# Kernel optimization log

Measured on AMD Instinct MI355X. Metric: run time of the kernel, lower is better.

The kernel has to match this reference:

```python
import jax, jax.numpy as jnp
import numpy as np

BATCH = 1048576
D_IN = 4        # d_in=3 spatial dims + 1 time dim
HID = 64
N_HID_STACK = 4  # hidden residual blocks after the first hidden layer
D_OUT = 3
BN_EPS = 1e-5


def _bn(x, gamma, beta):
    # BatchNorm1d in training mode: biased batch statistics over the batch axis
    mu = jnp.mean(x, axis=0)
    var = jnp.var(x, axis=0)
    return gamma * (x - mu) * jax.lax.rsqrt(var + BN_EPS) + beta


def setup_inputs() -> dict:
    key = jax.random.key(0)
    ks = jax.random.split(key, 8)
    s_in = 1.0 / np.sqrt(D_IN)
    s_h = 1.0 / np.sqrt(HID)
    return {
        "x": jax.random.normal(ks[0], (BATCH, D_IN), dtype=jnp.float32),
        "bn0_gamma": jnp.ones((D_IN,), jnp.float32),
        "bn0_beta": jnp.zeros((D_IN,), jnp.float32),
        "W0": jax.random.normal(ks[1], (D_IN, HID), jnp.float32) * s_in,
        "b0": jnp.zeros((HID,), jnp.float32),
        "gamma0": jnp.ones((HID,), jnp.float32),
        "beta0": jnp.zeros((HID,), jnp.float32),
        "W_hid": jax.random.normal(ks[2], (N_HID_STACK, HID, HID), jnp.float32) * s_h,
        "b_hid": jnp.zeros((N_HID_STACK, HID), jnp.float32),
        "gamma_hid": jnp.ones((N_HID_STACK, HID), jnp.float32),
        "beta_hid": jnp.zeros((N_HID_STACK, HID), jnp.float32),
        "Wout": jax.random.normal(ks[3], (HID, D_OUT), jnp.float32) * s_h,
        "bout": jnp.zeros((D_OUT,), jnp.float32),
    }


def reference(x, bn0_gamma, bn0_beta, W0, b0, gamma0, beta0,
              W_hid, b_hid, gamma_hid, beta_hid, Wout, bout):
    # Net.forward (u-network, single patch, batch_normalization=True, tanh):
    #   x = bn0(x)
    #   y = bn(act(Linear0(x)))                 (first hidden layer, no skip)
    #   y = bn_i(act(Linear_i(y))) + y          (residual hidden layers)
    #   y = Linear_out(y)
    h = _bn(x, bn0_gamma, bn0_beta)
    y = _bn(jnp.tanh(h @ W0 + b0), gamma0, beta0)

    def step(y, layer):
        W, b, g, be = layer
        return _bn(jnp.tanh(y @ W + b), g, be) + y, None

    y, _ = jax.lax.scan(step, y, (W_hid, b_hid, gamma_hid, beta_hid))
    return y @ Wout + bout
```

## Files before the change

kernel.cpp:

```cpp
#include <hip/hip_runtime.h>
#include <stdint.h>


#define NROWS 1048576
#define EPS 1e-5f
#define INV_B 9.5367431640625e-07f
#define LOG2E2 2.885390081777927f
#define TILES 4
#define BIGGRID 2048

typedef __attribute__((ext_vector_type(8))) short bfrag;
typedef __attribute__((ext_vector_type(4))) float facc;
typedef __attribute__((ext_vector_type(4))) float f4v;

__device__ __forceinline__ float bf2f(short s) {
  union { unsigned u; float f; } v;
  v.u = ((unsigned)(unsigned short)s) << 16;
  return v.f;
}
__device__ __forceinline__ short f2bf(float f) {
  union { float f; unsigned u; } v;
  v.f = f;
  unsigned r = v.u + 0x7FFFu + ((v.u >> 16) & 1u);
  return (short)(r >> 16);
}
__device__ __forceinline__ float tanh_fast(float x) {
  float e = __builtin_amdgcn_exp2f(x * LOG2E2);
  return 1.f - 2.f * __builtin_amdgcn_rcpf(e + 1.f);
}

template <int W>
__global__ __launch_bounds__(256) void k_reduce(const float* __restrict__ P,
                                                float* __restrict__ S,
                                                int rows_per_blk) {
  __shared__ float red[256];
  const int tid = threadIdx.x;
  const int col = tid % W;
  const int grp = tid / W;
  const int G = 256 / W;
  size_t r0 = (size_t)blockIdx.x * rows_per_blk;
  float s = 0.f;
  for (int r = grp; r < rows_per_blk; r += G) s += P[(r0 + r) * W + col];
  red[tid] = s;
  __syncthreads();
  if (tid < W) {
    float t = 0.f;
#pragma unroll 4
    for (int g = 0; g < G; ++g) t += red[g * W + tid];
    atomicAdd(&S[tid], t);
  }
}


__global__ __launch_bounds__(256) void k_stats_x(const float* __restrict__ x,
                                                 float* __restrict__ P) {
  __shared__ float red[4][8];
  const int tid = threadIdx.x;
  const int wave = tid >> 6;
  size_t base = (size_t)blockIdx.x * 1024 + tid;
  float s[4] = {0.f, 0.f, 0.f, 0.f}, q[4] = {0.f, 0.f, 0.f, 0.f};
#pragma unroll
  for (int it = 0; it < 4; ++it) {
    f4v v = *(const f4v*)(x + (base + (size_t)it * 256) * 4);
#pragma unroll
    for (int k = 0; k < 4; ++k) { s[k] += v[k]; q[k] = fmaf(v[k], v[k], q[k]); }
  }
#pragma unroll
  for (int off = 32; off > 0; off >>= 1) {
#pragma unroll
    for (int k = 0; k < 4; ++k) {
      s[k] += __shfl_xor(s[k], off);
      q[k] += __shfl_xor(q[k], off);
    }
  }
  if ((tid & 63) == 0) {
#pragma unroll
    for (int k = 0; k < 4; ++k) { red[wave][k] = s[k]; red[wave][4 + k] = q[k]; }
  }
  __syncthreads();
  if (tid < 8)
    P[blockIdx.x * 8 + tid] =
        red[0][tid] + red[1][tid] + red[2][tid] + red[3][tid];
}

__global__ __launch_bounds__(256) void k_stats_z1(
    const float* __restrict__ x, const float* __restrict__ bn0g,
    const float* __restrict__ bn0b, const float* __restrict__ W0,
    const float* __restrict__ b0, const float* __restrict__ sx,
    float* __restrict__ P) {
  __shared__ float red[2][4][64];
  const int tid = threadIdx.x;
  const int lane = tid & 63;
  const int wave = tid >> 6;
  int gw = blockIdx.x * 4 + wave;
  float sc[4], sh[4];
#pragma unroll
  for (int k = 0; k < 4; ++k) {
    float mean = sx[k] * INV_B;
    float var = fmaf(-mean, mean, sx[4 + k] * INV_B);
    float rs = rsqrtf(var + EPS);
    sc[k] = bn0g[k] * rs;
    sh[k] = fmaf(-sc[k], mean, bn0b[k]);
  }
  float w[4];
#pragma unroll
  for (int k = 0; k < 4; ++k) w[k] = W0[k * 64 + lane];
  float bj = b0[lane];
  float s = 0.f, q = 0.f;
  size_t r0 = (size_t)gw * 256;
  for (int r = 0; r < 256; ++r) {
    f4v xv = *(const f4v*)(x + (r0 + r) * 4);
    float acc = bj;
#pragma unroll
    for (int k = 0; k < 4; ++k)
      acc = fmaf(fmaf(xv[k], sc[k], sh[k]), w[k], acc);
    float z = tanh_fast(acc);
    s += z;
    q = fmaf(z, z, q);
  }
  red[0][wave][lane] = s;
  red[1][wave][lane] = q;
  __syncthreads();
  if (tid < 128) {
    int which = tid >> 6, c = tid & 63;
    P[blockIdx.x * 128 + tid] = red[which][0][c] + red[which][1][c] +
                                red[which][2][c] + red[which][3][c];
  }
}

__global__ __launch_bounds__(256) void k_prep(const float* __restrict__ Wh,
                                              short* __restrict__ WT) {
  int idx = blockIdx.x * 256 + threadIdx.x;
  int l = idx >> 12, rem = idx & 4095, k = rem >> 6, c = rem & 63;
  WT[l * 4096 + c * 64 + k] = f2bf(Wh[l * 4096 + k * 64 + c]);
}


__global__ __launch_bounds__(256, 3) void k_first(
    const float* __restrict__ x, const float* __restrict__ bn0g,
    const float* __restrict__ bn0b, const float* __restrict__ W0,
    const float* __restrict__ b0, const float* __restrict__ gamma0,
    const float* __restrict__ beta0, const float* __restrict__ sx,
    const float* __restrict__ s1, const short* __restrict__ WTb,
    const float* __restrict__ bb, float* __restrict__ P,
    short* __restrict__ Y) {
  __shared__ __align__(16) float lds_x[128 * 4];
  __shared__ __align__(16) short lds_y[128 * 72];
  __shared__ float lds_st[128];

  const int tid = threadIdx.x;
  const int lane = tid & 63;
  const int wave = tid >> 6;
  const int l15 = lane & 15;
  const int q = lane >> 4;
  const int wr = wave * 32;

  if (tid < 128) lds_st[tid] = 0.f;
  float sc0[4], sh0[4];
#pragma unroll
  for (int k = 0; k < 4; ++k) {
    float mean = sx[k] * INV_B;
    float var = fmaf(-mean, mean, sx[4 + k] * INV_B);
    float rs = rsqrtf(var + EPS);
    sc0[k] = bn0g[k] * rs;
    sh0[k] = fmaf(-sc0[k], mean, bn0b[k]);
  }
  float w0c[4];
#pragma unroll
  for (int k = 0; k < 4; ++k) w0c[k] = W0[k * 64 + lane];
  float b0c = b0[lane];
  float mean1 = s1[lane] * INV_B;
  float var1 = fmaf(-mean1, mean1, s1[64 + lane] * INV_B);
  float A1c = gamma0[lane] * rsqrtf(var1 + EPS);
  float B1c = fmaf(-A1c, mean1, beta0[lane]);
  float bbv[4];
  bfrag bwb[4][2];
#pragma unroll
  for (int nt = 0; nt < 4; ++nt) {
    bbv[nt] = bb[nt * 16 + l15];
#pragma unroll
    for (int kt = 0; kt < 2; ++kt)
      bwb[nt][kt] =
          *(const bfrag*)(WTb + (nt * 16 + l15) * 64 + kt * 32 + q * 8);
  }
  __syncthreads();

  float sAcc[4] = {0.f, 0.f, 0.f, 0.f}, qAcc[4] = {0.f, 0.f, 0.f, 0.f};
  const size_t tbase = (size_t)blockIdx.x * TILES * 128;

  f4v xp;
  if (lane < 32) xp = *(const f4v*)(x + (tbase + wr + lane) * 4);

#pragma unroll
  for (int t = 0; t < TILES; ++t) {
    const size_t r0 = tbase + (size_t)t * 128;
    if (lane < 32) *(f4v*)&lds_x[(wr + lane) * 4] = xp;
    if (t + 1 < TILES && lane < 32)
      xp = *(const f4v*)(x + (r0 + 128 + wr + lane) * 4);

    for (int e = 0; e < 32; ++e) {
      int row = wr + e;
      float acc = b0c;
#pragma unroll
      for (int k = 0; k < 4; ++k)
        acc = fmaf(fmaf(lds_x[row * 4 + k], sc0[k], sh0[k]), w0c[k], acc);
      float z = tanh_fast(acc);
      lds_y[row * 72 + lane] = f2bf(fmaf(A1c, z, B1c));
    }

    bfrag af[2][2];
#pragma unroll
    for (int mt = 0; mt < 2; ++mt)
#pragma unroll
      for (int kt = 0; kt < 2; ++kt) {
        af[mt][kt] =
            *(const bfrag*)&lds_y[(wr + mt * 16 + l15) * 72 + kt * 32 + q * 8];
        *(bfrag*)(Y + (r0 + wr + mt * 16 + l15) * 64 + kt * 32 + q * 8) =
            af[mt][kt];
      }
    facc acc2[2][4];
#pragma unroll
    for (int mt = 0; mt < 2; ++mt)
#pragma unroll
      for (int nt = 0; nt < 4; ++nt) {
        acc2[mt][nt][0] = bbv[nt]; acc2[mt][nt][1] = bbv[nt];
        acc2[mt][nt][2] = bbv[nt]; acc2[mt][nt][3] = bbv[nt];
      }
#pragma unroll
    for (int mt = 0; mt < 2; ++mt)
#pragma unroll
      for (int nt = 0; nt < 4; ++nt)
#pragma unroll
        for (int kt = 0; kt < 2; ++kt)
          acc2[mt][nt] = __builtin_amdgcn_mfma_f32_16x16x32_bf16(
              af[mt][kt], bwb[nt][kt], acc2[mt][nt], 0, 0, 0);
#pragma unroll
    for (int nt = 0; nt < 4; ++nt)
#pragma unroll
      for (int mt = 0; mt < 2; ++mt)
#pragma unroll
        for (int i = 0; i < 4; ++i) {
          float z = tanh_fast(acc2[mt][nt][i]);
          sAcc[nt] += z;
          qAcc[nt] = fmaf(z, z, qAcc[nt]);
        }
  }

#pragma unroll
  for (int nt = 0; nt < 4; ++nt) {
    float s = sAcc[nt], ss = qAcc[nt];
    s += __shfl_xor(s, 16); s += __shfl_xor(s, 32);
    ss += __shfl_xor(ss, 16); ss += __shfl_xor(ss, 32);
    if (q == 0) {
      atomicAdd(&lds_st[nt * 16 + l15], s);
      atomicAdd(&lds_st[64 + nt * 16 + l15], ss);
    }
  }
  __syncthreads();
  if (tid < 128) P[(size_t)blockIdx.x * 128 + tid] = lds_st[tid];
}

__global__ __launch_bounds__(256, 3) void k_mid(
    short* __restrict__ Y, const short* __restrict__ WTa,
    const float* __restrict__ ba, const float* __restrict__ ga,
    const float* __restrict__ bea, const float* __restrict__ sa,
    const short* __restrict__ WTb, const float* __restrict__ bb,
    float* __restrict__ P) {
  __shared__ __align__(16) short lds_y[128 * 72];
  __shared__ float lds_st[128];

  const int tid = threadIdx.x;
  const int lane = tid & 63;
  const int wave = tid >> 6;
  const int l15 = lane & 15;
  const int q = lane >> 4;
  const int wr = wave * 32;

  if (tid < 128) lds_st[tid] = 0.f;
  float Av[4], Bv[4], bav[4], bbv[4];
#pragma unroll
  for (int nt = 0; nt < 4; ++nt) {
    int c = nt * 16 + l15;
    float mean = sa[c] * INV_B;
    float var = fmaf(-mean, mean, sa[64 + c] * INV_B);
    float A = ga[c] * rsqrtf(var + EPS);
    Av[nt] = A;
    Bv[nt] = fmaf(-A, mean, bea[c]);
    bav[nt] = ba[c];
    bbv[nt] = bb[c];
  }
  bfrag bwa[4][2], bwb[4][2];
#pragma unroll
  for (int nt = 0; nt < 4; ++nt)
#pragma unroll
    for (int kt = 0; kt < 2; ++kt) {
      bwa[nt][kt] =
          *(const bfrag*)(WTa + (nt * 16 + l15) * 64 + kt * 32 + q * 8);
      bwb[nt][kt] =
          *(const bfrag*)(WTb + (nt * 16 + l15) * 64 + kt * 32 + q * 8);
    }
  __syncthreads();

  float sAcc[4] = {0.f, 0.f, 0.f, 0.f}, qAcc[4] = {0.f, 0.f, 0.f, 0.f};
  const size_t tbase = (size_t)blockIdx.x * TILES * 128;
  const int srow = lane >> 3;
  const int sc8 = (lane & 7) * 8;

  bfrag ld[4];
  {
    const size_t g = (tbase + wr + srow) * 64 + sc8;
#pragma unroll
    for (int it = 0; it < 4; ++it)
      ld[it] = *(const bfrag*)(Y + g + (size_t)it * 8 * 64);
  }

#pragma unroll
  for (int t = 0; t < TILES; ++t) {
    const size_t r0 = tbase + (size_t)t * 128;
#pragma unroll
    for (int it = 0; it < 4; ++it)
      *(bfrag*)&lds_y[(wr + it * 8 + srow) * 72 + sc8] = ld[it];
    if (t + 1 < TILES) {
      const size_t g = (r0 + 128 + wr + srow) * 64 + sc8;
#pragma unroll
      for (int it = 0; it < 4; ++it)
        ld[it] = *(const bfrag*)(Y + g + (size_t)it * 8 * 64);
    }

    bfrag af[2][2];
#pragma unroll
    for (int mt = 0; mt < 2; ++mt)
#pragma unroll
      for (int kt = 0; kt < 2; ++kt)
        af[mt][kt] =
            *(const bfrag*)&lds_y[(wr + mt * 16 + l15) * 72 + kt * 32 + q * 8];
    facc acc[2][4];
#pragma unroll
    for (int mt = 0; mt < 2; ++mt)
#pragma unroll
      for (int nt = 0; nt < 4; ++nt) {
        acc[mt][nt][0] = bav[nt]; acc[mt][nt][1] = bav[nt];
        acc[mt][nt][2] = bav[nt]; acc[mt][nt][3] = bav[nt];
      }
#pragma unroll
    for (int mt = 0; mt < 2; ++mt)
#pragma unroll
      for (int nt = 0; nt < 4; ++nt)
#pragma unroll
        for (int kt = 0; kt < 2; ++kt)
          acc[mt][nt] = __builtin_amdgcn_mfma_f32_16x16x32_bf16(
              af[mt][kt], bwa[nt][kt], acc[mt][nt], 0, 0, 0);

#pragma unroll
    for (int mt = 0; mt < 2; ++mt)
#pragma unroll
      for (int nt = 0; nt < 4; ++nt) {
        int c = nt * 16 + l15;
        float A = Av[nt], Bc = Bv[nt];
#pragma unroll
        for (int i = 0; i < 4; ++i) {
          int rl = wr + mt * 16 + q * 4 + i;
          float z = tanh_fast(acc[mt][nt][i]);
          float yo = bf2f(lds_y[rl * 72 + c]);
          lds_y[rl * 72 + c] = f2bf(fmaf(A, z, Bc) + yo);
        }
      }

#pragma unroll
    for (int mt = 0; mt < 2; ++mt)
#pragma unroll
      for (int kt = 0; kt < 2; ++kt) {
        af[mt][kt] =
            *(const bfrag*)&lds_y[(wr + mt * 16 + l15) * 72 + kt * 32 + q * 8];
        *(bfrag*)(Y + (r0 + wr + mt * 16 + l15) * 64 + kt * 32 + q * 8) =
            af[mt][kt];
      }
#pragma unroll
    for (int mt = 0; mt < 2; ++mt)
#pragma unroll
      for (int nt = 0; nt < 4; ++nt) {
        acc[mt][nt][0] = bbv[nt]; acc[mt][nt][1] = bbv[nt];
        acc[mt][nt][2] = bbv[nt]; acc[mt][nt][3] = bbv[nt];
      }
#pragma unroll
    for (int mt = 0; mt < 2; ++mt)
#pragma unroll
      for (int nt = 0; nt < 4; ++nt)
#pragma unroll
        for (int kt = 0; kt < 2; ++kt)
          acc[mt][nt] = __builtin_amdgcn_mfma_f32_16x16x32_bf16(
              af[mt][kt], bwb[nt][kt], acc[mt][nt], 0, 0, 0);
#pragma unroll
    for (int nt = 0; nt < 4; ++nt)
#pragma unroll
      for (int mt = 0; mt < 2; ++mt)
#pragma unroll
        for (int i = 0; i < 4; ++i) {
          float z = tanh_fast(acc[mt][nt][i]);
          sAcc[nt] += z;
          qAcc[nt] = fmaf(z, z, qAcc[nt]);
        }
  }

#pragma unroll
  for (int nt = 0; nt < 4; ++nt) {
    float s = sAcc[nt], ss = qAcc[nt];
    s += __shfl_xor(s, 16); s += __shfl_xor(s, 32);
    ss += __shfl_xor(ss, 16); ss += __shfl_xor(ss, 32);
    if (q == 0) {
      atomicAdd(&lds_st[nt * 16 + l15], s);
      atomicAdd(&lds_st[64 + nt * 16 + l15], ss);
    }
  }
  __syncthreads();
  if (tid < 128) P[(size_t)blockIdx.x * 128 + tid] = lds_st[tid];
}

__global__ __launch_bounds__(256, 3) void k_last(
    const short* __restrict__ Y, const short* __restrict__ WTa,
    const float* __restrict__ ba, const float* __restrict__ ga,
    const float* __restrict__ bea, const float* __restrict__ sa,
    const float* __restrict__ Wout, const float* __restrict__ bout,
    float* __restrict__ out) {
  __shared__ __align__(16) short lds_y[128 * 72];
  __shared__ float lds_wo[192];

  const int tid = threadIdx.x;
  const int lane = tid & 63;
  const int wave = tid >> 6;
  const int l15 = lane & 15;
  const int q = lane >> 4;
  const int wr = wave * 32;

  if (tid < 192) lds_wo[tid] = Wout[tid];
  float Av[4], Bv[4], bav[4];
#pragma unroll
  for (int nt = 0; nt < 4; ++nt) {
    int c = nt * 16 + l15;
    float mean = sa[c] * INV_B;
    float var = fmaf(-mean, mean, sa[64 + c] * INV_B);
    float A = ga[c] * rsqrtf(var + EPS);
    Av[nt] = A;
    Bv[nt] = fmaf(-A, mean, bea[c]);
    bav[nt] = ba[c];
  }
  bfrag bwa[4][2];
#pragma unroll
  for (int nt = 0; nt < 4; ++nt)
#pragma unroll
    for (int kt = 0; kt < 2; ++kt)
      bwa[nt][kt] =
          *(const bfrag*)(WTa + (nt * 16 + l15) * 64 + kt * 32 + q * 8);
  float bo0 = bout[0], bo1 = bout[1], bo2 = bout[2];
  __syncthreads();

  const size_t tbase = (size_t)blockIdx.x * TILES * 128;
  const int srow = lane >> 3;
  const int sc8 = (lane & 7) * 8;

  bfrag ld[4];
  {
    const size_t g = (tbase + wr + srow) * 64 + sc8;
#pragma unroll
    for (int it = 0; it < 4; ++it)
      ld[it] = *(const bfrag*)(Y + g + (size_t)it * 8 * 64);
  }

#pragma unroll
  for (int t = 0; t < TILES; ++t) {
    const size_t r0 = tbase + (size_t)t * 128;
#pragma unroll
    for (int it = 0; it < 4; ++it)
      *(bfrag*)&lds_y[(wr + it * 8 + srow) * 72 + sc8] = ld[it];
    if (t + 1 < TILES) {
      const size_t g = (r0 + 128 + wr + srow) * 64 + sc8;
#pragma unroll
      for (int it = 0; it < 4; ++it)
        ld[it] = *(const bfrag*)(Y + g + (size_t)it * 8 * 64);
    }

    bfrag af[2][2];
#pragma unroll
    for (int mt = 0; mt < 2; ++mt)
#pragma unroll
      for (int kt = 0; kt < 2; ++kt)
        af[mt][kt] =
            *(const bfrag*)&lds_y[(wr + mt * 16 + l15) * 72 + kt * 32 + q * 8];
    facc acc[2][4];
#pragma unroll
    for (int mt = 0; mt < 2; ++mt)
#pragma unroll
      for (int nt = 0; nt < 4; ++nt) {
        acc[mt][nt][0] = bav[nt]; acc[mt][nt][1] = bav[nt];
        acc[mt][nt][2] = bav[nt]; acc[mt][nt][3] = bav[nt];
      }
#pragma unroll
    for (int mt = 0; mt < 2; ++mt)
#pragma unroll
      for (int nt = 0; nt < 4; ++nt)
#pragma unroll
        for (int kt = 0; kt < 2; ++kt)
          acc[mt][nt] = __builtin_amdgcn_mfma_f32_16x16x32_bf16(
              af[mt][kt], bwa[nt][kt], acc[mt][nt], 0, 0, 0);
#pragma unroll
    for (int mt = 0; mt < 2; ++mt)
#pragma unroll
      for (int nt = 0; nt < 4; ++nt) {
        int c = nt * 16 + l15;
        float A = Av[nt], Bc = Bv[nt];
#pragma unroll
        for (int i = 0; i < 4; ++i) {
          int rl = wr + mt * 16 + q * 4 + i;
          float z = tanh_fast(acc[mt][nt][i]);
          float yo = bf2f(lds_y[rl * 72 + c]);
          lds_y[rl * 72 + c] = f2bf(fmaf(A, z, Bc) + yo);
        }
      }

    {
      int row = wr + (lane >> 1);
      int cb = (lane & 1) * 32;
      float o0 = 0.f, o1 = 0.f, o2 = 0.f;
#pragma unroll
      for (int jc = 0; jc < 4; ++jc) {
        bfrag v = *(const bfrag*)&lds_y[row * 72 + cb + jc * 8];
#pragma unroll
        for (int j = 0; j < 8; ++j) {
          float f = bf2f(v[j]);
          int jj = cb + jc * 8 + j;
          o0 = fmaf(f, lds_wo[jj * 3 + 0], o0);
          o1 = fmaf(f, lds_wo[jj * 3 + 1], o1);
          o2 = fmaf(f, lds_wo[jj * 3 + 2], o2);
        }
      }
      o0 += __shfl_xor(o0, 1);
      o1 += __shfl_xor(o1, 1);
      o2 += __shfl_xor(o2, 1);
      if ((lane & 1) == 0) {
        size_t ro = (r0 + row) * 3;
        out[ro] = o0 + bo0;
        out[ro + 1] = o1 + bo1;
        out[ro + 2] = o2 + bo2;
      }
    }
  }
}

extern "C" void kernel_launch(void* const* d_in, const int* in_sizes, int n_in,
                              void* d_out, int out_size, void* d_ws,
                              size_t ws_size, hipStream_t stream) {
  (void)in_sizes; (void)n_in; (void)out_size; (void)ws_size;
  const float* x = (const float*)d_in[0];
  const float* bn0g = (const float*)d_in[1];
  const float* bn0b = (const float*)d_in[2];
  const float* W0 = (const float*)d_in[3];
  const float* b0 = (const float*)d_in[4];
  const float* gamma0 = (const float*)d_in[5];
  const float* beta0 = (const float*)d_in[6];
  const float* Wh = (const float*)d_in[7];
  const float* bh = (const float*)d_in[8];
  const float* gh = (const float*)d_in[9];
  const float* beh = (const float*)d_in[10];
  const float* Wout = (const float*)d_in[11];
  const float* bout = (const float*)d_in[12];
  float* out = (float*)d_out;

  char* ws = (char*)d_ws;
  short* Y = (short*)ws;
  const size_t YB = (size_t)NROWS * 64 * 2;
  float* stats = (float*)(ws + YB);
  float* Sx = stats;
  float* S1 = stats + 8;
  float* S2 = stats + 136;
  float* S3 = stats + 264;
  float* S4 = stats + 392;
  float* S5 = stats + 520;
  short* WT = (short*)(ws + YB + 4096);
  float* P = (float*)(ws + YB + 4096 + 32768);

  hipMemsetAsync(stats, 0, 648 * sizeof(float), stream);
  k_prep<<<64, 256, 0, stream>>>(Wh, WT);
  k_stats_x<<<1024, 256, 0, stream>>>(x, P);
  k_reduce<8><<<8, 256, 0, stream>>>(P, Sx, 128);
  k_stats_z1<<<1024, 256, 0, stream>>>(x, bn0g, bn0b, W0, b0, Sx, P);
  k_reduce<128><<<8, 256, 0, stream>>>(P, S1, 128);
  k_first<<<BIGGRID, 256, 0, stream>>>(x, bn0g, bn0b, W0, b0, gamma0, beta0,
                                       Sx, S1, WT, bh, P, Y);
  k_reduce<128><<<16, 256, 0, stream>>>(P, S2, 128);
  k_mid<<<BIGGRID, 256, 0, stream>>>(Y, WT, bh, gh, beh, S2, WT + 4096,
                                     bh + 64, P);
  k_reduce<128><<<16, 256, 0, stream>>>(P, S3, 128);
  k_mid<<<BIGGRID, 256, 0, stream>>>(Y, WT + 4096, bh + 64, gh + 64, beh + 64,
                                     S3, WT + 2 * 4096, bh + 128, P);
  k_reduce<128><<<16, 256, 0, stream>>>(P, S4, 128);
  k_mid<<<BIGGRID, 256, 0, stream>>>(Y, WT + 2 * 4096, bh + 128, gh + 128,
                                     beh + 128, S4, WT + 3 * 4096, bh + 192, P);
  k_reduce<128><<<16, 256, 0, stream>>>(P, S5, 128);
  k_last<<<BIGGRID, 256, 0, stream>>>(Y, WT + 3 * 4096, bh + 192, gh + 192,
                                      beh + 192, S5, Wout, bout, out);
}
```

Before: 600.1 us.

## Switch to one 64-row tile per block with many small blocks

Removes the per-block multi-tile loop and software prefetch, so each 128-thread block processes a single 64-row tile and the grid is 8x larger. Reduce kernels are launched with more blocks to handle the larger per-block partial-statistics buffer. This is meant to raise occupancy and latency hiding across CUs, at the cost of repeated per-block weight/parameter loads, more partial sums to reduce, and the loss of explicit load/compute overlap.

```diff
diff --git a/kernel.cpp b/kernel.cpp
--- a/kernel.cpp
+++ b/kernel.cpp
@@ -6,8 +6,7 @@
 #define EPS 1e-5f
 #define INV_B 9.5367431640625e-07f
 #define LOG2E2 2.885390081777927f
-#define TILES 4
-#define BIGGRID 2048
+#define BIGGRID 16384
 
 typedef __attribute__((ext_vector_type(8))) short bfrag;
 typedef __attribute__((ext_vector_type(4))) float facc;
@@ -136,7 +135,7 @@
 }
 
 
-__global__ __launch_bounds__(256, 3) void k_first(
+__global__ __launch_bounds__(128) void k_first(
     const float* __restrict__ x, const float* __restrict__ bn0g,
     const float* __restrict__ bn0b, const float* __restrict__ W0,
     const float* __restrict__ b0, const float* __restrict__ gamma0,
@@ -144,8 +143,8 @@
     const float* __restrict__ s1, const short* __restrict__ WTb,
     const float* __restrict__ bb, float* __restrict__ P,
     short* __restrict__ Y) {
-  __shared__ __align__(16) float lds_x[128 * 4];
-  __shared__ __align__(16) short lds_y[128 * 72];
+  __shared__ __align__(16) float lds_x[64 * 4];
+  __shared__ __align__(16) short lds_y[64 * 72];
   __shared__ float lds_st[128];
 
   const int tid = threadIdx.x;
@@ -154,8 +153,12 @@
   const int l15 = lane & 15;
   const int q = lane >> 4;
   const int wr = wave * 32;
-
-  if (tid < 128) lds_st[tid] = 0.f;
+  const size_t r0 = (size_t)blockIdx.x * 64;
+
+  f4v xp;
+  if (lane < 32) xp = *(const f4v*)(x + (r0 + wr + lane) * 4);
+
+  lds_st[tid] = 0.f;
   float sc0[4], sh0[4];
 #pragma unroll
   for (int k = 0; k < 4; ++k) {
@@ -173,6 +176,29 @@
   float var1 = fmaf(-mean1, mean1, s1[64 + lane] * INV_B);
   float A1c = gamma0[lane] * rsqrtf(var1 + EPS);
   float B1c = fmaf(-A1c, mean1, beta0[lane]);
+  if (lane < 32) *(f4v*)&lds_x[(wr + lane) * 4] = xp;
+  __syncthreads();
+
+  for (int e = 0; e < 32; ++e) {
+    int row = wr + e;
+    float acc = b0c;
+#pragma unroll
+    for (int k = 0; k < 4; ++k)
+      acc = fmaf(fmaf(lds_x[row * 4 + k], sc0[k], sh0[k]), w0c[k], acc);
+    float z = tanh_fast(acc);
+    lds_y[row * 72 + lane] = f2bf(fmaf(A1c, z, B1c));
+  }
+
+  bfrag af[2][2];
+#pragma unroll
+  for (int mt = 0; mt < 2; ++mt)
+#pragma unroll
+    for (int kt = 0; kt < 2; ++kt) {
+      af[mt][kt] =
+          *(const bfrag*)&lds_y[(wr + mt * 16 + l15) * 72 + kt * 32 + q * 8];
+      *(bfrag*)(Y + (r0 + wr + mt * 16 + l15) * 64 + kt * 32 + q * 8) =
+          af[mt][kt];
+    }
   float bbv[4];
   bfrag bwb[4][2];
 #pragma unroll
@@ -183,71 +209,35 @@
       bwb[nt][kt] =
           *(const bfrag*)(WTb + (nt * 16 + l15) * 64 + kt * 32 + q * 8);
   }
-  __syncthreads();
-
-  float sAcc[4] = {0.f, 0.f, 0.f, 0.f}, qAcc[4] = {0.f, 0.f, 0.f, 0.f};
-  const size_t tbase = (size_t)blockIdx.x * TILES * 128;
-
-  f4v xp;
-  if (lane < 32) xp = *(const f4v*)(x + (tbase + wr + lane) * 4);
-
-#pragma unroll
-  for (int t = 0; t < TILES; ++t) {
-    const size_t r0 = tbase + (size_t)t * 128;
-    if (lane < 32) *(f4v*)&lds_x[(wr + lane) * 4] = xp;
-    if (t + 1 < TILES && lane < 32)
-      xp = *(const f4v*)(x + (r0 + 128 + wr + lane) * 4);
-
-    for (int e = 0; e < 32; ++e) {
-      int row = wr + e;
-      float acc = b0c;
-#pragma unroll
-      for (int k = 0; k < 4; ++k)
-        acc = fmaf(fmaf(lds_x[row * 4 + k], sc0[k], sh0[k]), w0c[k], acc);
-      float z = tanh_fast(acc);
-      lds_y[row * 72 + lane] = f2bf(fmaf(A1c, z, B1c));
-    }
-
-    bfrag af[2][2];
+  facc acc2[2][4];
+#pragma unroll
+  for (int mt = 0; mt < 2; ++mt)
+#pragma unroll
+    for (int nt = 0; nt < 4; ++nt) {
+      acc2[mt][nt][0] = bbv[nt]; acc2[mt][nt][1] = bbv[nt];
+      acc2[mt][nt][2] = bbv[nt]; acc2[mt][nt][3] = bbv[nt];
+    }
+#pragma unroll
+  for (int mt = 0; mt < 2; ++mt)
+#pragma unroll
+    for (int nt = 0; nt < 4; ++nt)
+#pragma unroll
+      for (int kt = 0; kt < 2; ++kt)
+        acc2[mt][nt] = __builtin_amdgcn_mfma_f32_16x16x32_bf16(
+            af[mt][kt], bwb[nt][kt], acc2[mt][nt], 0, 0, 0);
+  float sAcc[4], qAcc[4];
+#pragma unroll
+  for (int nt = 0; nt < 4; ++nt) {
+    sAcc[nt] = 0.f;
+    qAcc[nt] = 0.f;
 #pragma unroll
     for (int mt = 0; mt < 2; ++mt)
 #pragma unroll
-      for (int kt = 0; kt < 2; ++kt) {
-        af[mt][kt] =
-            *(const bfrag*)&lds_y[(wr + mt * 16 + l15) * 72 + kt * 32 + q * 8];
-        *(bfrag*)(Y + (r0 + wr + mt * 16 + l15) * 64 + kt * 32 + q * 8) =
-            af[mt][kt];
+      for (int i = 0; i < 4; ++i) {
+        float z = tanh_fast(acc2[mt][nt][i]);
+        sAcc[nt] += z;
+        qAcc[nt] = fmaf(z, z, qAcc[nt]);
       }
-    facc acc2[2][4];
-#pragma unroll
-    for (int mt = 0; mt < 2; ++mt)
-#pragma unroll
-      for (int nt = 0; nt < 4; ++nt) {
-        acc2[mt][nt][0] = bbv[nt]; acc2[mt][nt][1] = bbv[nt];
-        acc2[mt][nt][2] = bbv[nt]; acc2[mt][nt][3] = bbv[nt];
-      }
-#pragma unroll
-    for (int mt = 0; mt < 2; ++mt)
-#pragma unroll
-      for (int nt = 0; nt < 4; ++nt)
-#pragma unroll
-        for (int kt = 0; kt < 2; ++kt)
-          acc2[mt][nt] = __builtin_amdgcn_mfma_f32_16x16x32_bf16(
-              af[mt][kt], bwb[nt][kt], acc2[mt][nt], 0, 0, 0);
-#pragma unroll
-    for (int nt = 0; nt < 4; ++nt)
-#pragma unroll
-      for (int mt = 0; mt < 2; ++mt)
-#pragma unroll
-        for (int i = 0; i < 4; ++i) {
-          float z = tanh_fast(acc2[mt][nt][i]);
-          sAcc[nt] += z;
-          qAcc[nt] = fmaf(z, z, qAcc[nt]);
-        }
-  }
-
-#pragma unroll
-  for (int nt = 0; nt < 4; ++nt) {
     float s = sAcc[nt], ss = qAcc[nt];
     s += __shfl_xor(s, 16); s += __shfl_xor(s, 32);
     ss += __shfl_xor(ss, 16); ss += __shfl_xor(ss, 32);
@@ -257,16 +247,16 @@
     }
   }
   __syncthreads();
-  if (tid < 128) P[(size_t)blockIdx.x * 128 + tid] = lds_st[tid];
-}
-
-__global__ __launch_bounds__(256, 3) void k_mid(
+  P[(size_t)blockIdx.x * 128 + tid] = lds_st[tid];
+}
+
+__global__ __launch_bounds__(128) void k_mid(
     short* __restrict__ Y, const short* __restrict__ WTa,
     const float* __restrict__ ba, const float* __restrict__ ga,
     const float* __restrict__ bea, const float* __restrict__ sa,
     const short* __restrict__ WTb, const float* __restrict__ bb,
     float* __restrict__ P) {
-  __shared__ __align__(16) short lds_y[128 * 72];
+  __shared__ __align__(16) short lds_y[64 * 72];
   __shared__ float lds_st[128];
 
   const int tid = threadIdx.x;
@@ -275,9 +265,20 @@
   const int l15 = lane & 15;
   const int q = lane >> 4;
   const int wr = wave * 32;
-
-  if (tid < 128) lds_st[tid] = 0.f;
-  float Av[4], Bv[4], bav[4], bbv[4];
+  const size_t r0 = (size_t)blockIdx.x * 64;
+  const int srow = lane >> 3;
+  const int sc8 = (lane & 7) * 8;
+
+  bfrag ld[4];
+  {
+    const size_t g = (r0 + wr + srow) * 64 + sc8;
+#pragma unroll
+    for (int it = 0; it < 4; ++it)
+      ld[it] = *(const bfrag*)(Y + g + (size_t)it * 8 * 64);
+  }
+
+  lds_st[tid] = 0.f;
+  float Av[4], Bv[4], bav[4];
 #pragma unroll
   for (int nt = 0; nt < 4; ++nt) {
     int c = nt * 16 + l15;
@@ -287,124 +288,104 @@
     Av[nt] = A;
     Bv[nt] = fmaf(-A, mean, bea[c]);
     bav[nt] = ba[c];
-    bbv[nt] = bb[c];
-  }
-  bfrag bwa[4][2], bwb[4][2];
+  }
+  bfrag bwa[4][2];
 #pragma unroll
   for (int nt = 0; nt < 4; ++nt)
 #pragma unroll
-    for (int kt = 0; kt < 2; ++kt) {
+    for (int kt = 0; kt < 2; ++kt)
       bwa[nt][kt] =
           *(const bfrag*)(WTa + (nt * 16 + l15) * 64 + kt * 32 + q * 8);
+
+#pragma unroll
+  for (int it = 0; it < 4; ++it)
+    *(bfrag*)&lds_y[(wr + it * 8 + srow) * 72 + sc8] = ld[it];
+  __syncthreads();
+
+  bfrag af[2][2];
+#pragma unroll
+  for (int mt = 0; mt < 2; ++mt)
+#pragma unroll
+    for (int kt = 0; kt < 2; ++kt)
+      af[mt][kt] =
+          *(const bfrag*)&lds_y[(wr + mt * 16 + l15) * 72 + kt * 32 + q * 8];
+  facc acc[2][4];
+#pragma unroll
+  for (int mt = 0; mt < 2; ++mt)
+#pragma unroll
+    for (int nt = 0; nt < 4; ++nt) {
+      acc[mt][nt][0] = bav[nt]; acc[mt][nt][1] = bav[nt];
+      acc[mt][nt][2] = bav[nt]; acc[mt][nt][3] = bav[nt];
+    }
+#pragma unroll
+  for (int mt = 0; mt < 2; ++mt)
+#pragma unroll
+    for (int nt = 0; nt < 4; ++nt)
+#pragma unroll
+      for (int kt = 0; kt < 2; ++kt)
+        acc[mt][nt] = __builtin_amdgcn_mfma_f32_16x16x32_bf16(
+            af[mt][kt], bwa[nt][kt], acc[mt][nt], 0, 0, 0);
+
+#pragma unroll
+  for (int mt = 0; mt < 2; ++mt)
+#pragma unroll
+    for (int nt = 0; nt < 4; ++nt) {
+      int c = nt * 16 + l15;
+      float A = Av[nt], Bc = Bv[nt];
+#pragma unroll
+      for (int i = 0; i < 4; ++i) {
+        int rl = wr + mt * 16 + q * 4 + i;
+        float z = tanh_fast(acc[mt][nt][i]);
+        float yo = bf2f(lds_y[rl * 72 + c]);
+        lds_y[rl * 72 + c] = f2bf(fmaf(A, z, Bc) + yo);
+      }
+    }
+
+#pragma unroll
+  for (int mt = 0; mt < 2; ++mt)
+#pragma unroll
+    for (int kt = 0; kt < 2; ++kt) {
+      af[mt][kt] =
+          *(const bfrag*)&lds_y[(wr + mt * 16 + l15) * 72 + kt * 32 + q * 8];
+      *(bfrag*)(Y + (r0 + wr + mt * 16 + l15) * 64 + kt * 32 + q * 8) =
+          af[mt][kt];
+    }
+  float bbv[4];
+  bfrag bwb[4][2];
+#pragma unroll
+  for (int nt = 0; nt < 4; ++nt) {
+    bbv[nt] = bb[nt * 16 + l15];
+#pragma unroll
+    for (int kt = 0; kt < 2; ++kt)
       bwb[nt][kt] =
           *(const bfrag*)(WTb + (nt * 16 + l15) * 64 + kt * 32 + q * 8);
-    }
-  __syncthreads();
-
-  float sAcc[4] = {0.f, 0.f, 0.f, 0.f}, qAcc[4] = {0.f, 0.f, 0.f, 0.f};
-  const size_t tbase = (size_t)blockIdx.x * TILES * 128;
-  const int srow = lane >> 3;
-  const int sc8 = (lane & 7) * 8;
-
-  bfrag ld[4];
-  {
-    const size_t g = (tbase + wr + srow) * 64 + sc8;
-#pragma unroll
-    for (int it = 0; it < 4; ++it)
-      ld[it] = *(const bfrag*)(Y + g + (size_t)it * 8 * 64);
-  }
-
-#pragma unroll
-  for (int t = 0; t < TILES; ++t) {
-    const size_t r0 = tbase + (size_t)t * 128;
-#pragma unroll
-    for (int it = 0; it < 4; ++it)
-      *(bfrag*)&lds_y[(wr + it * 8 + srow) * 72 + sc8] = ld[it];
-    if (t + 1 < TILES) {
-      const size_t g = (r0 + 128 + wr + srow) * 64 + sc8;
-#pragma unroll
-      for (int it = 0; it < 4; ++it)
-        ld[it] = *(const bfrag*)(Y + g + (size_t)it * 8 * 64);
-    }
-
-    bfrag af[2][2];
+  }
+#pragma unroll
+  for (int mt = 0; mt < 2; ++mt)
+#pragma unroll
+    for (int nt = 0; nt < 4; ++nt) {
+      acc[mt][nt][0] = bbv[nt]; acc[mt][nt][1] = bbv[nt];
+      acc[mt][nt][2] = bbv[nt]; acc[mt][nt][3] = bbv[nt];
+    }
+#pragma unroll
+  for (int mt = 0; mt < 2; ++mt)
+#pragma unroll
+    for (int nt = 0; nt < 4; ++nt)
+#pragma unroll
+      for (int kt = 0; kt < 2; ++kt)
+        acc[mt][nt] = __builtin_amdgcn_mfma_f32_16x16x32_bf16(
+            af[mt][kt], bwb[nt][kt], acc[mt][nt], 0, 0, 0);
+#pragma unroll
+  for (int nt = 0; nt < 4; ++nt) {
+    float s = 0.f, ss = 0.f;
 #pragma unroll
     for (int mt = 0; mt < 2; ++mt)
 #pragma unroll
-      for (int kt = 0; kt < 2; ++kt)
-        af[mt][kt] =
-            *(const bfrag*)&lds_y[(wr + mt * 16 + l15) * 72 + kt * 32 + q * 8];
-    facc acc[2][4];
-#pragma unroll
-    for (int mt = 0; mt < 2; ++mt)
-#pragma unroll
-      for (int nt = 0; nt < 4; ++nt) {
-        acc[mt][nt][0] = bav[nt]; acc[mt][nt][1] = bav[nt];
-        acc[mt][nt][2] = bav[nt]; acc[mt][nt][3] = bav[nt];
+      for (int i = 0; i < 4; ++i) {
+        float z = tanh_fast(acc[mt][nt][i]);
+        s += z;
+        ss = fmaf(z, z, ss);
       }
-#pragma unroll
-    for (int mt = 0; mt < 2; ++mt)
-#pragma unroll
-      for (int nt = 0; nt < 4; ++nt)
-#pragma unroll
-        for (int kt = 0; kt < 2; ++kt)
-          acc[mt][nt] = __builtin_amdgcn_mfma_f32_16x16x32_bf16(
-              af[mt][kt], bwa[nt][kt], acc[mt][nt], 0, 0, 0);
-
-#pragma unroll
-    for (int mt = 0; mt < 2; ++mt)
-#pragma unroll
-      for (int nt = 0; nt < 4; ++nt) {
-        int c = nt * 16 + l15;
-        float A = Av[nt], Bc = Bv[nt];
-#pragma unroll
-        for (int i = 0; i < 4; ++i) {
-          int rl = wr + mt * 16 + q * 4 + i;
-          float z = tanh_fast(acc[mt][nt][i]);
-          float yo = bf2f(lds_y[rl * 72 + c]);
-          lds_y[rl * 72 + c] = f2bf(fmaf(A, z, Bc) + yo);
-        }
-      }
-
-#pragma unroll
-    for (int mt = 0; mt < 2; ++mt)
-#pragma unroll
-      for (int kt = 0; kt < 2; ++kt) {
-        af[mt][kt] =
-            *(const bfrag*)&lds_y[(wr + mt * 16 + l15) * 72 + kt * 32 + q * 8];
-        *(bfrag*)(Y + (r0 + wr + mt * 16 + l15) * 64 + kt * 32 + q * 8) =
-            af[mt][kt];
-      }
-#pragma unroll
-    for (int mt = 0; mt < 2; ++mt)
-#pragma unroll
-      for (int nt = 0; nt < 4; ++nt) {
-        acc[mt][nt][0] = bbv[nt]; acc[mt][nt][1] = bbv[nt];
-        acc[mt][nt][2] = bbv[nt]; acc[mt][nt][3] = bbv[nt];
-      }
-#pragma unroll
-    for (int mt = 0; mt < 2; ++mt)
-#pragma unroll
-      for (int nt = 0; nt < 4; ++nt)
-#pragma unroll
-        for (int kt = 0; kt < 2; ++kt)
-          acc[mt][nt] = __builtin_amdgcn_mfma_f32_16x16x32_bf16(
-              af[mt][kt], bwb[nt][kt], acc[mt][nt], 0, 0, 0);
-#pragma unroll
-    for (int nt = 0; nt < 4; ++nt)
-#pragma unroll
-      for (int mt = 0; mt < 2; ++mt)
-#pragma unroll
-        for (int i = 0; i < 4; ++i) {
-          float z = tanh_fast(acc[mt][nt][i]);
-          sAcc[nt] += z;
-          qAcc[nt] = fmaf(z, z, qAcc[nt]);
-        }
-  }
-
-#pragma unroll
-  for (int nt = 0; nt < 4; ++nt) {
-    float s = sAcc[nt], ss = qAcc[nt];
     s += __shfl_xor(s, 16); s += __shfl_xor(s, 32);
     ss += __shfl_xor(ss, 16); ss += __shfl_xor(ss, 32);
     if (q == 0) {
@@ -413,16 +394,16 @@
     }
   }
   __syncthreads();
-  if (tid < 128) P[(size_t)blockIdx.x * 128 + tid] = lds_st[tid];
-}
-
-__global__ __launch_bounds__(256, 3) void k_last(
+  P[(size_t)blockIdx.x * 128 + tid] = lds_st[tid];
+}
+
+__global__ __launch_bounds__(128) void k_last(
     const short* __restrict__ Y, const short* __restrict__ WTa,
     const float* __restrict__ ba, const float* __restrict__ ga,
     const float* __restrict__ bea, const float* __restrict__ sa,
     const float* __restrict__ Wout, const float* __restrict__ bout,
     float* __restrict__ out) {
-  __shared__ __align__(16) short lds_y[128 * 72];
+  __shared__ __align__(16) short lds_y[64 * 72];
   __shared__ float lds_wo[192];
 
   const int tid = threadIdx.x;
@@ -431,8 +412,19 @@
   const int l15 = lane & 15;
   const int q = lane >> 4;
   const int wr = wave * 32;
-
-  if (tid < 192) lds_wo[tid] = Wout[tid];
+  const size_t r0 = (size_t)blockIdx.x * 64;
+  const int srow = lane >> 3;
+  const int sc8 = (lane & 7) * 8;
+
+  bfrag ld[4];
+  {
+    const size_t g = (r0 + wr + srow) * 64 + sc8;
+#pragma unroll
+    for (int it = 0; it < 4; ++it)
+      ld[it] = *(const bfrag*)(Y + g + (size_t)it * 8 * 64);
+  }
+
+  for (int i = tid; i < 192; i += 128) lds_wo[i] = Wout[i];
   float Av[4], Bv[4], bav[4];
 #pragma unroll
   for (int nt = 0; nt < 4; ++nt) {
@@ -452,96 +444,74 @@
       bwa[nt][kt] =
           *(const bfrag*)(WTa + (nt * 16 + l15) * 64 + kt * 32 + q * 8);
   float bo0 = bout[0], bo1 = bout[1], bo2 = bout[2];
-  __syncthreads();
-
-  const size_t tbase = (size_t)blockIdx.x * TILES * 128;
-  const int srow = lane >> 3;
-  const int sc8 = (lane & 7) * 8;
-
-  bfrag ld[4];
+
+#pragma unroll
+  for (int it = 0; it < 4; ++it)
+    *(bfrag*)&lds_y[(wr + it * 8 + srow) * 72 + sc8] = ld[it];
+  __syncthreads();
+
+  bfrag af[2][2];
+#pragma unroll
+  for (int mt = 0; mt < 2; ++mt)
+#pragma unroll
+    for (int kt = 0; kt < 2; ++kt)
+      af[mt][kt] =
+          *(const bfrag*)&lds_y[(wr + mt * 16 + l15) * 72 + kt * 32 + q * 8];
+  facc acc[2][4];
+#pragma unroll
+  for (int mt = 0; mt < 2; ++mt)
+#pragma unroll
+    for (int nt = 0; nt < 4; ++nt) {
+      acc[mt][nt][0] = bav[nt]; acc[mt][nt][1] = bav[nt];
+      acc[mt][nt][2] = bav[nt]; acc[mt][nt][3] = bav[nt];
+    }
+#pragma unroll
+  for (int mt = 0; mt < 2; ++mt)
+#pragma unroll
+    for (int nt = 0; nt < 4; ++nt)
+#pragma unroll
+      for (int kt = 0; kt < 2; ++kt)
+        acc[mt][nt] = __builtin_amdgcn_mfma_f32_16x16x32_bf16(
+            af[mt][kt], bwa[nt][kt], acc[mt][nt], 0, 0, 0);
+#pragma unroll
+  for (int mt = 0; mt < 2; ++mt)
+#pragma unroll
+    for (int nt = 0; nt < 4; ++nt) {
+      int c = nt * 16 + l15;
+      float A = Av[nt], Bc = Bv[nt];
+#pragma unroll
+      for (int i = 0; i < 4; ++i) {
+        int rl = wr + mt * 16 + q * 4 + i;
+        float z = tanh_fast(acc[mt][nt][i]);
+        float yo = bf2f(lds_y[rl * 72 + c]);
+        lds_y[rl * 72 + c] = f2bf(fmaf(A, z, Bc) + yo);
+      }
+    }
+
   {
-    const size_t g = (tbase + wr + srow) * 64 + sc8;
-#pragma unroll
-    for (int it = 0; it < 4; ++it)
-      ld[it] = *(const bfrag*)(Y + g + (size_t)it * 8 * 64);
-  }
-
-#pragma unroll
-  for (int t = 0; t < TILES; ++t) {
-    const size_t r0 = tbase + (size_t)t * 128;
-#pragma unroll
-    for (int it = 0; it < 4; ++it)
-      *(bfrag*)&lds_y[(wr + it * 8 + srow) * 72 + sc8] = ld[it];
-    if (t + 1 < TILES) {
-      const size_t g = (r0 + 128 + wr + srow) * 64 + sc8;
-#pragma unroll
-      for (int it = 0; it < 4; ++it)
-        ld[it] = *(const bfrag*)(Y + g + (size_t)it * 8 * 64);
-    }
-
-    bfrag af[2][2];
-#pragma unroll
-    for (int mt = 0; mt < 2; ++mt)
-#pragma unroll
-      for (int kt = 0; kt < 2; ++kt)
-        af[mt][kt] =
-            *(const bfrag*)&lds_y[(wr + mt * 16 + l15) * 72 + kt * 32 + q * 8];
-    facc acc[2][4];
-#pragma unroll
-    for (int mt = 0; mt < 2; ++mt)
-#pragma unroll
-      for (int nt = 0; nt < 4; ++nt) {
-        acc[mt][nt][0] = bav[nt]; acc[mt][nt][1] = bav[nt];
-        acc[mt][nt][2] = bav[nt]; acc[mt][nt][3] = bav[nt];
+    int row = wr + (lane >> 1);
+    int cb = (lane & 1) * 32;
+    float o0 = 0.f, o1 = 0.f, o2 = 0.f;
+#pragma unroll
+    for (int jc = 0; jc < 4; ++jc) {
+      bfrag v = *(const bfrag*)&lds_y[row * 72 + cb + jc * 8];
+#pragma unroll
+      for (int j = 0; j < 8; ++j) {
+        float f = bf2f(v[j]);
+        int jj = cb + jc * 8 + j;
+        o0 = fmaf(f, lds_wo[jj * 3 + 0], o0);
+        o1 = fmaf(f, lds_wo[jj * 3 + 1], o1);
+        o2 = fmaf(f, lds_wo[jj * 3 + 2], o2);
       }
-#pragma unroll
-    for (int mt = 0; mt < 2; ++mt)
-#pragma unroll
-      for (int nt = 0; nt < 4; ++nt)
-#pragma unroll
-        for (int kt = 0; kt < 2; ++kt)
-          acc[mt][nt] = __builtin_amdgcn_mfma_f32_16x16x32_bf16(
-              af[mt][kt], bwa[nt][kt], acc[mt][nt], 0, 0, 0);
-#pragma unroll
-    for (int mt = 0; mt < 2; ++mt)
-#pragma unroll
-      for (int nt = 0; nt < 4; ++nt) {
-        int c = nt * 16 + l15;
-        float A = Av[nt], Bc = Bv[nt];
-#pragma unroll
-        for (int i = 0; i < 4; ++i) {
-          int rl = wr + mt * 16 + q * 4 + i;
-          float z = tanh_fast(acc[mt][nt][i]);
-          float yo = bf2f(lds_y[rl * 72 + c]);
-          lds_y[rl * 72 + c] = f2bf(fmaf(A, z, Bc) + yo);
-        }
-      }
-
-    {
-      int row = wr + (lane >> 1);
-      int cb = (lane & 1) * 32;
-      float o0 = 0.f, o1 = 0.f, o2 = 0.f;
-#pragma unroll
-      for (int jc = 0; jc < 4; ++jc) {
-        bfrag v = *(const bfrag*)&lds_y[row * 72 + cb + jc * 8];
-#pragma unroll
-        for (int j = 0; j < 8; ++j) {
-          float f = bf2f(v[j]);
-          int jj = cb + jc * 8 + j;
-          o0 = fmaf(f, lds_wo[jj * 3 + 0], o0);
-          o1 = fmaf(f, lds_wo[jj * 3 + 1], o1);
-          o2 = fmaf(f, lds_wo[jj * 3 + 2], o2);
-        }
-      }
-      o0 += __shfl_xor(o0, 1);
-      o1 += __shfl_xor(o1, 1);
-      o2 += __shfl_xor(o2, 1);
-      if ((lane & 1) == 0) {
-        size_t ro = (r0 + row) * 3;
-        out[ro] = o0 + bo0;
-        out[ro + 1] = o1 + bo1;
-        out[ro + 2] = o2 + bo2;
-      }
+    }
+    o0 += __shfl_xor(o0, 1);
+    o1 += __shfl_xor(o1, 1);
+    o2 += __shfl_xor(o2, 1);
+    if ((lane & 1) == 0) {
+      size_t ro = (r0 + row) * 3;
+      out[ro] = o0 + bo0;
+      out[ro + 1] = o1 + bo1;
+      out[ro + 2] = o2 + bo2;
     }
   }
 }
@@ -584,18 +554,18 @@
   k_reduce<8><<<8, 256, 0, stream>>>(P, Sx, 128);
   k_stats_z1<<<1024, 256, 0, stream>>>(x, bn0g, bn0b, W0, b0, Sx, P);
   k_reduce<128><<<8, 256, 0, stream>>>(P, S1, 128);
-  k_first<<<BIGGRID, 256, 0, stream>>>(x, bn0g, bn0b, W0, b0, gamma0, beta0,
+  k_first<<<BIGGRID, 128, 0, stream>>>(x, bn0g, bn0b, W0, b0, gamma0, beta0,
                                        Sx, S1, WT, bh, P, Y);
-  k_reduce<128><<<16, 256, 0, stream>>>(P, S2, 128);
-  k_mid<<<BIGGRID, 256, 0, stream>>>(Y, WT, bh, gh, beh, S2, WT + 4096,
+  k_reduce<128><<<128, 256, 0, stream>>>(P, S2, 128);
+  k_mid<<<BIGGRID, 128, 0, stream>>>(Y, WT, bh, gh, beh, S2, WT + 4096,
                                      bh + 64, P);
-  k_reduce<128><<<16, 256, 0, stream>>>(P, S3, 128);
-  k_mid<<<BIGGRID, 256, 0, stream>>>(Y, WT + 4096, bh + 64, gh + 64, beh + 64,
+  k_reduce<128><<<128, 256, 0, stream>>>(P, S3, 128);
+  k_mid<<<BIGGRID, 128, 0, stream>>>(Y, WT + 4096, bh + 64, gh + 64, beh + 64,
                                      S3, WT + 2 * 4096, bh + 128, P);
-  k_reduce<128><<<16, 256, 0, stream>>>(P, S4, 128);
-  k_mid<<<BIGGRID, 256, 0, stream>>>(Y, WT + 2 * 4096, bh + 128, gh + 128,
+  k_reduce<128><<<128, 256, 0, stream>>>(P, S4, 128);
+  k_mid<<<BIGGRID, 128, 0, stream>>>(Y, WT + 2 * 4096, bh + 128, gh + 128,
                                      beh + 128, S4, WT + 3 * 4096, bh + 192, P);
-  k_reduce<128><<<16, 256, 0, stream>>>(P, S5, 128);
-  k_last<<<BIGGRID, 256, 0, stream>>>(Y, WT + 3 * 4096, bh + 192, gh + 192,
+  k_reduce<128><<<128, 256, 0, stream>>>(P, S5, 128);
+  k_last<<<BIGGRID, 128, 0, stream>>>(Y, WT + 3 * 4096, bh + 192, gh + 192,
                                       beh + 192, S5, Wout, bout, out);
 }
```

Measured after the change: 562.4 us. 1.07x faster.
